# Kernel tuning notes

Measured on AMD Instinct MI355X. Metric: run time of the kernel, lower is better.

## Reference

```python
import jax, jax.numpy as jnp
import numpy as np


def binarize_det(t):
    # Torch Binarize 'det': ((t - 0.5).sign() + 1) / 2  -> values in {0, 0.5, 1}
    return (jnp.sign(t - 0.5) + 1.0) * 0.5


def setup_inputs() -> dict:
    key = jax.random.key(0)
    k1, k2, k3 = jax.random.split(key, 3)
    B = 262144
    x = jax.random.uniform(k1, (B, 1, 1, 120), dtype=jnp.float32)
    # BNNConv2d(1, 120, kernel_size=(1,120)): weight [out=120, in=1, kh=1, kw=120],
    # init uniform(0,1) per init_w
    conv_w = jax.random.uniform(k2, (120, 1, 1, 120), dtype=jnp.float32)
    # BNNLinear(120, num_classes=1): weight [1, 120], init ~N(0.5, 0.01) per init_w
    lin_w = 0.5 + 0.01 * jax.random.normal(k3, (1, 120), dtype=jnp.float32)
    return {"x": x, "conv_w": conv_w, "lin_w": lin_w}


def reference(x, conv_w, lin_w):
    B = x.shape[0]
    # Binarize input and conv weight
    xb = binarize_det(x)          # [B,1,1,120]
    wb = binarize_det(conv_w)     # [120,1,1,120]
    # conv2d with kernel (1,120) on input [B,1,1,120] collapses to a GEMM:
    # out[b,o] = sum_k xb[b,0,0,k] * wb[o,0,0,k]
    y = jnp.einsum('bk,ok->bo', xb.reshape(B, 120), wb.reshape(120, 120))  # [B,120]
    # Softsign
    s = y / (1.0 + jnp.abs(y))
    # Flatten is identity on [B,120]; BNNLinear binarizes its input and weight, no bias
    sb = binarize_det(s)
    lwb = binarize_det(lin_w)     # [num_classes,120]
    out = jnp.einsum('bk,ck->bc', sb, lwb)  # [B,num_classes]
    return out
```

## Files before the change

### kernel.cpp

```cpp
#include <hip/hip_runtime.h>
#include <hip/hip_bf16.h>

typedef __attribute__((ext_vector_type(8))) short short8;
typedef __attribute__((ext_vector_type(4))) float floatx4;

__device__ __forceinline__ short bin_bf16s(float v) {
    float d = v - 0.5f;
    return (d > 0.f) ? (short)0x3F80 : ((d < 0.f) ? (short)0 : (short)0x3F00);
}
__device__ __forceinline__ float bin_f32(float v) {
    float d = v - 0.5f;
    return (d > 0.f) ? 1.f : ((d < 0.f) ? 0.f : 0.5f);
}

__global__ void prep_w(const float* __restrict__ w, unsigned short* __restrict__ wb) {
    int g  = blockIdx.x * 256 + threadIdx.x;
    int n  = g >> 4;
    int gi = g & 15;
    int k0 = gi * 8;
    short8 v = {0, 0, 0, 0, 0, 0, 0, 0};
    if (n < 120 && gi < 15) {
        const float* p = w + n * 120 + k0;
        floatx4 f0 = *(const floatx4*)p;
        floatx4 f1 = *(const floatx4*)(p + 4);
        #pragma unroll
        for (int j = 0; j < 4; ++j) { v[j] = bin_bf16s(f0[j]); v[4 + j] = bin_bf16s(f1[j]); }
    }
    int byte = (n * 256 + k0 * 2) ^ ((n & 7) << 4);
    *(short8*)((char*)wb + byte) = v;
}

__global__ __launch_bounds__(256) void bnn_main(
    const float* __restrict__ x, const unsigned short* __restrict__ wbs,
    const float* __restrict__ lin_w, float* __restrict__ out)
{
    __shared__ unsigned short W[16384];

    const int tid = threadIdx.x;
    {
        const floatx4* src = (const floatx4*)wbs;
        floatx4*       dst = (floatx4*)W;
        #pragma unroll
        for (int i = 0; i < 8; ++i) dst[tid + i * 256] = src[tid + i * 256];
    }
    __syncthreads();

    const int wave = tid >> 6;
    const int lane = tid & 63;
    const int cl   = lane & 15;
    const int q    = lane >> 4;
    const long row0 = (long)blockIdx.x * 128 + (long)wave * 32;

    float lw[8];
    #pragma unroll
    for (int t = 0; t < 8; ++t) {
        int c = t * 16 + cl;
        lw[t] = (c < 120) ? bin_f32(lin_w[c]) : 0.f;
    }

    floatx4 acc[2][8];
    const floatx4 z4 = {0.f, 0.f, 0.f, 0.f};
    #pragma unroll
    for (int rt = 0; rt < 2; ++rt)
        #pragma unroll
        for (int t = 0; t < 8; ++t) acc[rt][t] = z4;

    const char* Wb = (const char*)W;
    const float* rp0 = x + (row0 + cl) * 120;
    const float* rp1 = x + (row0 + 16 + cl) * 120;

    #pragma unroll
    for (int s = 0; s < 4; ++s) {
        short8 af[2];
        #pragma unroll
        for (int rt = 0; rt < 2; ++rt) {
            short8 a = {0, 0, 0, 0, 0, 0, 0, 0};
            if (!(s == 3 && q == 3)) {
                const float* p = (rt == 0 ? rp0 : rp1) + s * 32 + q * 8;
                floatx4 f0 = *(const floatx4*)p;
                floatx4 f1 = *(const floatx4*)(p + 4);
                #pragma unroll
                for (int j = 0; j < 4; ++j) { a[j] = bin_bf16s(f0[j]); a[4 + j] = bin_bf16s(f1[j]); }
            }
            af[rt] = a;
        }
        #pragma unroll
        for (int t = 0; t < 8; ++t) {
            int n = t * 16 + cl;
            int byte = (n * 256 + (s * 32 + q * 8) * 2) ^ ((n & 7) << 4);
            short8 bf = *(const short8*)(Wb + byte);
            acc[0][t] = __builtin_amdgcn_mfma_f32_16x16x32_bf16(af[0], bf, acc[0][t], 0, 0, 0);
            acc[1][t] = __builtin_amdgcn_mfma_f32_16x16x32_bf16(af[1], bf, acc[1][t], 0, 0, 0);
        }
    }

    #pragma unroll
    for (int rt = 0; rt < 2; ++rt) {
        float p4[4] = {0.f, 0.f, 0.f, 0.f};
        #pragma unroll
        for (int t = 0; t < 8; ++t)
            #pragma unroll
            for (int j = 0; j < 4; ++j) {
                float y  = acc[rt][t][j];
                float sb = (y > 1.f) ? 1.f : ((y == 1.f) ? 0.5f : 0.f);
                p4[j] += sb * lw[t];
            }
        #pragma unroll
        for (int m = 1; m <= 8; m <<= 1)
            #pragma unroll
            for (int j = 0; j < 4; ++j) p4[j] += __shfl_xor(p4[j], m, 64);
        if (cl == 0) {
            #pragma unroll
            for (int j = 0; j < 4; ++j)
                out[row0 + rt * 16 + q * 4 + j] = p4[j];
        }
    }
}

extern "C" void kernel_launch(void* const* d_in, const int* in_sizes, int n_in,
                              void* d_out, int out_size, void* d_ws, size_t ws_size,
                              hipStream_t stream) {
    const float* x      = (const float*)d_in[0];
    const float* conv_w = (const float*)d_in[1];
    const float* lin_w  = (const float*)d_in[2];
    float*       out    = (float*)d_out;
    unsigned short* wbs = (unsigned short*)d_ws;

    prep_w<<<dim3(8), dim3(256), 0, stream>>>(conv_w, wbs);

    const int B = in_sizes[0] / 120;
    bnn_main<<<dim3(B / 128), dim3(256), 0, stream>>>(x, wbs, lin_w, out);
}
```

Measured before the change: 192.4 us.

## Replace bf16 MFMA GEMM with bit-packed popcount BNN kernel fused with weight prep

Drops the separate weight-binarization kernel and the bf16 MFMA path. Each block now packs the binarized conv weights into bitmasks in shared memory, and each thread packs its own input row into bitmasks. Dot products become popcount over ANDed masks, with a fast path that assumes no exact-0.5 values and a slower four-term fallback for the 0.5 case. Each thread handles one row with 30 vector loads held in registers. This reduces LDS traffic and instruction count, but every block redoes the weight packing, and strided per-thread row loads may coalesce poorly.

```diff
diff --git a/kernel.cpp b/kernel.cpp
--- a/kernel.cpp
+++ b/kernel.cpp
@@ -1,120 +1,119 @@
 #include <hip/hip_runtime.h>
-#include <hip/hip_bf16.h>
 
-typedef __attribute__((ext_vector_type(8))) short short8;
-typedef __attribute__((ext_vector_type(4))) float floatx4;
+typedef float floatx4 __attribute__((ext_vector_type(4)));
 
-__device__ __forceinline__ short bin_bf16s(float v) {
-    float d = v - 0.5f;
-    return (d > 0.f) ? (short)0x3F80 : ((d < 0.f) ? (short)0 : (short)0x3F00);
-}
-__device__ __forceinline__ float bin_f32(float v) {
-    float d = v - 0.5f;
-    return (d > 0.f) ? 1.f : ((d < 0.f) ? 0.f : 0.5f);
-}
-
-__global__ void prep_w(const float* __restrict__ w, unsigned short* __restrict__ wb) {
-    int g  = blockIdx.x * 256 + threadIdx.x;
-    int n  = g >> 4;
-    int gi = g & 15;
-    int k0 = gi * 8;
-    short8 v = {0, 0, 0, 0, 0, 0, 0, 0};
-    if (n < 120 && gi < 15) {
-        const float* p = w + n * 120 + k0;
-        floatx4 f0 = *(const floatx4*)p;
-        floatx4 f1 = *(const floatx4*)(p + 4);
-        #pragma unroll
-        for (int j = 0; j < 4; ++j) { v[j] = bin_bf16s(f0[j]); v[4 + j] = bin_bf16s(f1[j]); }
-    }
-    int byte = (n * 256 + k0 * 2) ^ ((n & 7) << 4);
-    *(short8*)((char*)wb + byte) = v;
-}
-
-__global__ __launch_bounds__(256) void bnn_main(
-    const float* __restrict__ x, const unsigned short* __restrict__ wbs,
-    const float* __restrict__ lin_w, float* __restrict__ out)
+__global__ __launch_bounds__(256) void bnn_fused(
+    const float* __restrict__ x, const float* __restrict__ w,
+    const float* __restrict__ lin_w, float* __restrict__ out, int B)
 {
-    __shared__ unsigned short W[16384];
+    __shared__ __attribute__((aligned(16))) unsigned int T[1088];
 
     const int tid = threadIdx.x;
+    const long r  = (long)blockIdx.x * 256 + tid;
+    const long rr = (r < B) ? r : (long)B - 1;
+
+    const floatx4* xr = (const floatx4*)(x + rr * 120);
+    floatx4 buf[15];
+    #pragma unroll
+    for (int g = 0; g < 15; ++g) buf[g] = xr[g];
+
+    unsigned int myvl = 0u;
+    if (tid < 240) {
+        const int c = tid >> 1, h = tid & 1;
+        const floatx4* wr = (const floatx4*)(w + c * 120 + h * 64);
+        unsigned int vh[2] = {0u, 0u}, vl[2] = {0u, 0u};
+        const int ng = h ? 14 : 16;
+        #pragma unroll
+        for (int g = 0; g < 16; ++g) {
+            if (g < ng) {
+                floatx4 f = wr[g];
+                #pragma unroll
+                for (int j = 0; j < 4; ++j) {
+                    const int kl = 4 * g + j;
+                    const int wd = kl >> 5, sh = kl & 31;
+                    float d = 0.5f - f[j];
+                    unsigned int du = __float_as_uint(d);
+                    vh[wd] |= (du >> 31) << sh;
+                    vl[wd] |= (du == 0u) ? (1u << sh) : 0u;
+                }
+            }
+        }
+        T[c * 4 + 2 * h]           = vh[0];
+        T[c * 4 + 2 * h + 1]       = vh[1];
+        T[480 + c * 4 + 2 * h]     = vl[0];
+        T[480 + c * 4 + 2 * h + 1] = vl[1];
+        myvl = vl[0] | vl[1];
+        if (h == 0) {
+            float d = 0.5f - lin_w[c];
+            unsigned int du = __float_as_uint(d);
+            float hlw = (du >> 31) ? 0.5f : ((du == 0u) ? 0.25f : 0.0f);
+            T[960 + c] = __float_as_uint(hlw);
+        }
+    }
     {
-        const floatx4* src = (const floatx4*)wbs;
-        floatx4*       dst = (floatx4*)W;
-        #pragma unroll
-        for (int i = 0; i < 8; ++i) dst[tid + i * 256] = src[tid + i * 256];
+        int wany = __any((int)(myvl != 0u));
+        if ((tid & 63) == 0) T[1081 + (tid >> 6)] = (unsigned int)wany;
     }
     __syncthreads();
 
-    const int wave = tid >> 6;
-    const int lane = tid & 63;
-    const int cl   = lane & 15;
-    const int q    = lane >> 4;
-    const long row0 = (long)blockIdx.x * 128 + (long)wave * 32;
+    floatx4 buf2[15];
+    #pragma unroll
+    for (int g = 0; g < 15; ++g) buf2[g] = xr[15 + g];
 
-    float lw[8];
+    unsigned int uh[4] = {0u,0u,0u,0u}, ul[4] = {0u,0u,0u,0u};
     #pragma unroll
-    for (int t = 0; t < 8; ++t) {
-        int c = t * 16 + cl;
-        lw[t] = (c < 120) ? bin_f32(lin_w[c]) : 0.f;
+    for (int g = 0; g < 15; ++g) {
+        #pragma unroll
+        for (int j = 0; j < 4; ++j) {
+            const int k = 4 * g + j, wd = k >> 5, sh = k & 31;
+            float d = 0.5f - buf[g][j];
+            unsigned int du = __float_as_uint(d);
+            uh[wd] |= (du >> 31) << sh;
+            ul[wd] |= (du == 0u) ? (1u << sh) : 0u;
+        }
     }
-
-    floatx4 acc[2][8];
-    const floatx4 z4 = {0.f, 0.f, 0.f, 0.f};
     #pragma unroll
-    for (int rt = 0; rt < 2; ++rt)
+    for (int g = 0; g < 15; ++g) {
         #pragma unroll
-        for (int t = 0; t < 8; ++t) acc[rt][t] = z4;
-
-    const char* Wb = (const char*)W;
-    const float* rp0 = x + (row0 + cl) * 120;
-    const float* rp1 = x + (row0 + 16 + cl) * 120;
-
-    #pragma unroll
-    for (int s = 0; s < 4; ++s) {
-        short8 af[2];
-        #pragma unroll
-        for (int rt = 0; rt < 2; ++rt) {
-            short8 a = {0, 0, 0, 0, 0, 0, 0, 0};
-            if (!(s == 3 && q == 3)) {
-                const float* p = (rt == 0 ? rp0 : rp1) + s * 32 + q * 8;
-                floatx4 f0 = *(const floatx4*)p;
-                floatx4 f1 = *(const floatx4*)(p + 4);
-                #pragma unroll
-                for (int j = 0; j < 4; ++j) { a[j] = bin_bf16s(f0[j]); a[4 + j] = bin_bf16s(f1[j]); }
-            }
-            af[rt] = a;
-        }
-        #pragma unroll
-        for (int t = 0; t < 8; ++t) {
-            int n = t * 16 + cl;
-            int byte = (n * 256 + (s * 32 + q * 8) * 2) ^ ((n & 7) << 4);
-            short8 bf = *(const short8*)(Wb + byte);
-            acc[0][t] = __builtin_amdgcn_mfma_f32_16x16x32_bf16(af[0], bf, acc[0][t], 0, 0, 0);
-            acc[1][t] = __builtin_amdgcn_mfma_f32_16x16x32_bf16(af[1], bf, acc[1][t], 0, 0, 0);
+        for (int j = 0; j < 4; ++j) {
+            const int k = 60 + 4 * g + j, wd = k >> 5, sh = k & 31;
+            float d = 0.5f - buf2[g][j];
+            unsigned int du = __float_as_uint(d);
+            uh[wd] |= (du >> 31) << sh;
+            ul[wd] |= (du == 0u) ? (1u << sh) : 0u;
         }
     }
 
-    #pragma unroll
-    for (int rt = 0; rt < 2; ++rt) {
-        float p4[4] = {0.f, 0.f, 0.f, 0.f};
-        #pragma unroll
-        for (int t = 0; t < 8; ++t)
-            #pragma unroll
-            for (int j = 0; j < 4; ++j) {
-                float y  = acc[rt][t][j];
-                float sb = (y > 1.f) ? 1.f : ((y == 1.f) ? 0.5f : 0.f);
-                p4[j] += sb * lw[t];
-            }
-        #pragma unroll
-        for (int m = 1; m <= 8; m <<= 1)
-            #pragma unroll
-            for (int j = 0; j < 4; ++j) p4[j] += __shfl_xor(p4[j], m, 64);
-        if (cl == 0) {
-            #pragma unroll
-            for (int j = 0; j < 4; ++j)
-                out[row0 + rt * 16 + q * 4 + j] = p4[j];
+    const unsigned int flagW = T[1081] | T[1082] | T[1083] | T[1084];
+    const bool rare = ((ul[0] | ul[1] | ul[2] | ul[3]) != 0u) || (flagW != 0u);
+
+    float acc = 0.0f;
+    const float* hlwt = (const float*)&T[960];
+    if (!__any((int)rare)) {
+        #pragma unroll 4
+        for (int c = 0; c < 120; ++c) {
+            const uint4 v = *(const uint4*)&T[c * 4];
+            int p =  __popc(v.x & uh[0]);
+            p    +=  __popc(v.y & uh[1]);
+            p    +=  __popc(v.z & uh[2]);
+            p    +=  __popc(v.w & uh[3]);
+            acc = fmaf((float)min(p, 2), hlwt[c], acc);
+        }
+    } else {
+        #pragma unroll 2
+        for (int c = 0; c < 120; ++c) {
+            const uint4 a = *(const uint4*)&T[c * 4];
+            const uint4 b = *(const uint4*)&T[480 + c * 4];
+            int phh = __popc(a.x & uh[0]) + __popc(a.y & uh[1]) + __popc(a.z & uh[2]) + __popc(a.w & uh[3]);
+            int phl = __popc(b.x & uh[0]) + __popc(b.y & uh[1]) + __popc(b.z & uh[2]) + __popc(b.w & uh[3]);
+            int plh = __popc(a.x & ul[0]) + __popc(a.y & ul[1]) + __popc(a.z & ul[2]) + __popc(a.w & ul[3]);
+            int pll = __popc(b.x & ul[0]) + __popc(b.y & ul[1]) + __popc(b.z & ul[2]) + __popc(b.w & ul[3]);
+            int S = 4 * phh + 2 * (phl + plh) + pll;
+            int t = (S >= 4 ? 1 : 0) + (S > 4 ? 1 : 0);
+            acc = fmaf((float)t, hlwt[c], acc);
         }
     }
+    if (r < B) out[r] = acc;
 }
 
 extern "C" void kernel_launch(void* const* d_in, const int* in_sizes, int n_in,
@@ -124,10 +123,8 @@
     const float* conv_w = (const float*)d_in[1];
     const float* lin_w  = (const float*)d_in[2];
     float*       out    = (float*)d_out;
-    unsigned short* wbs = (unsigned short*)d_ws;
-
-    prep_w<<<dim3(8), dim3(256), 0, stream>>>(conv_w, wbs);
 
     const int B = in_sizes[0] / 120;
-    bnn_main<<<dim3(B / 128), dim3(256), 0, stream>>>(x, wbs, lin_w, out);
+    const int blocks = (B + 255) / 256;
+    bnn_fused<<<dim3(blocks), dim3(256), 0, stream>>>(x, conv_w, lin_w, out, B);
 }
```

Result: slower. 199.6 us (+3.7%).
